# Kernel tuning notes

Hardware: AMD Instinct MI355X
Metric: run time of the kernel (lower is better)

Reference implementation:

```python
import jax, jax.numpy as jnp
import numpy as np

B, S, H = 2, 2048, 2048
NH, NKV, HD = 16, 4, 128
ROPE_BASE = 10000.0


def setup_inputs() -> dict:
    key = jax.random.key(0)
    ks = jax.random.split(key, 5)
    x = jax.random.normal(ks[0], (B, S, H), dtype=jnp.float32)
    position_ids = jnp.arange(S, dtype=jnp.int64 if jax.config.jax_enable_x64 else jnp.int32).reshape(1, S)
    # Linear weights stored as [in, out] (equivalent to torch weight.T)
    sc = 1.0 / np.sqrt(H)
    Wq = jax.random.normal(ks[1], (H, NH * HD), dtype=jnp.float32) * sc
    Wk = jax.random.normal(ks[2], (H, NKV * HD), dtype=jnp.float32) * sc
    Wv = jax.random.normal(ks[3], (H, NKV * HD), dtype=jnp.float32) * sc
    Wo = jax.random.normal(ks[4], (NH * HD, H), dtype=jnp.float32) * (1.0 / np.sqrt(NH * HD))
    return {"x": x, "position_ids": position_ids, "Wq": Wq, "Wk": Wk, "Wv": Wv, "Wo": Wo}


def _rope(q, k, position_ids):
    # q: [B,S,NH,HD], k: [B,S,NKV,HD]; Llama-style half-split RoPE
    half = HD // 2
    inv_freq = 1.0 / (ROPE_BASE ** (jnp.arange(0, half, dtype=jnp.float32) * 2.0 / HD))
    ang = position_ids.astype(jnp.float32)[..., None] * inv_freq  # [b,S,half]
    cos = jnp.concatenate([jnp.cos(ang), jnp.cos(ang)], axis=-1)[:, :, None, :]  # [b,S,1,HD]
    sin = jnp.concatenate([jnp.sin(ang), jnp.sin(ang)], axis=-1)[:, :, None, :]

    def rot_half(t):
        t1, t2 = t[..., :half], t[..., half:]
        return jnp.concatenate([-t2, t1], axis=-1)

    return q * cos + rot_half(q) * sin, k * cos + rot_half(k) * sin


def reference(x, position_ids, Wq, Wk, Wv, Wo):
    b, s, _ = x.shape
    q = (x @ Wq).reshape(b, s, NH, HD)
    k = (x @ Wk).reshape(b, s, NKV, HD)
    v = (x @ Wv).reshape(b, s, NKV, HD)
    q, k = _rope(q, k, position_ids)
    reps = NH // NKV
    k = jnp.repeat(k, reps, axis=2)  # repeat_interleave on head dim
    v = jnp.repeat(v, reps, axis=2)
    q = q.transpose(0, 2, 1, 3)  # [b,h,s,d]
    k = k.transpose(0, 2, 1, 3)
    v = v.transpose(0, 2, 1, 3)
    scores = jnp.einsum('bhqd,bhkd->bhqk', q, k) / jnp.sqrt(jnp.float32(HD))
    causal = jnp.triu(jnp.ones((s, s), dtype=bool), k=1)
    scores = jnp.where(causal, -jnp.inf, scores)
    attn = jax.nn.softmax(scores.astype(jnp.float32), axis=-1).astype(q.dtype)
    out = jnp.einsum('bhqk,bhkd->bhqd', attn, v)
    out = out.transpose(0, 2, 1, 3).reshape(b, s, NH * HD)
    return out @ Wo
```

## Files before the change

### kernel.cpp

```cpp
#include <hip/hip_runtime.h>
#include <stdint.h>

typedef unsigned short u16;
typedef __attribute__((ext_vector_type(8))) short short8;
typedef __attribute__((ext_vector_type(4))) float floatx4;

#define S_LEN 2048
#define NQKV 3072

#if __has_builtin(__builtin_amdgcn_exp2f)
#define EXP2F __builtin_amdgcn_exp2f
#else
#define EXP2F exp2f
#endif

__device__ inline float bf2f(u16 u) {
  union { uint32_t u; float f; } v; v.u = ((uint32_t)u) << 16; return v.f;
}
__device__ inline u16 f2bf(float f) {
  union { float f; uint32_t u; } v; v.f = f;
  uint32_t r = v.u + 0x7fffu + ((v.u >> 16) & 1u);
  return (u16)(r >> 16);
}
__device__ inline void gl2lds16(const u16* g, u16* l) {
  __builtin_amdgcn_global_load_lds((const __attribute__((address_space(1))) uint32_t*)g,
                                   (__attribute__((address_space(3))) uint32_t*)l, 16, 0, 0);
}

__global__ void cast_k(const float* __restrict__ in, u16* __restrict__ out, int n4) {
  int i = blockIdx.x * 256 + threadIdx.x;
  if (i >= n4) return;
  float4 v = ((const float4*)in)[i];
  ushort4 o;
  o.x = f2bf(v.x); o.y = f2bf(v.y); o.z = f2bf(v.z); o.w = f2bf(v.w);
  ((ushort4*)out)[i] = o;
}

__global__ void transpose_k(const float* __restrict__ in, u16* __restrict__ out, int K, int N) {
  __shared__ u16 tile[32][33];
  int n0 = blockIdx.x * 32, k0 = blockIdx.y * 32;
  int tx = threadIdx.x, ty = threadIdx.y;
#pragma unroll
  for (int i = 0; i < 4; i++)
    tile[ty + 8 * i][tx] = f2bf(in[(size_t)(k0 + ty + 8 * i) * N + n0 + tx]);
  __syncthreads();
#pragma unroll
  for (int i = 0; i < 4; i++)
    out[(size_t)(n0 + ty + 8 * i) * K + k0 + tx] = tile[tx][ty + 8 * i];
}

__global__ void vtrans_k(const u16* __restrict__ qkv, u16* __restrict__ vt) {
  __shared__ u16 tile[32][33];
  int bk = blockIdx.x * 32, bd = blockIdx.y * 32, bz = blockIdx.z;
  int bb = bz >> 2, kvh = bz & 3;
  const u16* src = qkv + ((size_t)bb * S_LEN) * NQKV + 2560 + kvh * 128;
  u16* dst = vt + (size_t)bz * 128 * 2048;
  int tx = threadIdx.x, ty = threadIdx.y;
#pragma unroll
  for (int i = 0; i < 4; i++)
    tile[ty + 8 * i][tx] = src[(size_t)(bk + ty + 8 * i) * NQKV + bd + tx];
  __syncthreads();
#pragma unroll
  for (int i = 0; i < 4; i++)
    dst[(size_t)(bd + ty + 8 * i) * 2048 + bk + tx] = tile[tx][ty + 8 * i];
}

template <bool OUTF32>
__global__ __launch_bounds__(256) void gemm_bt(const u16* __restrict__ A, const u16* __restrict__ Bt,
                                               void* __restrict__ Cv, int M, int N, int K) {
  __shared__ u16 As[128 * 32];
  __shared__ u16 Bs[128 * 32];
  const int m0 = blockIdx.y * 128, n0 = blockIdx.x * 128;
  const int t = threadIdx.x, w = t >> 6, lane = t & 63;
  const int quad = lane >> 4, l16 = lane & 15;
  const int wm = (w >> 1) * 64, wn = (w & 1) * 64;
  const int lrow = lane >> 2, lk = (lane & 3) * 8;
  floatx4 acc[4][4] = {};
  for (int k0 = 0; k0 < K; k0 += 32) {
#pragma unroll
    for (int c = 2 * w; c <= 2 * w + 1; ++c) {
      int row = c * 16 + lrow;
      gl2lds16(A + (size_t)(m0 + row) * K + k0 + lk, As + c * 512 + lane * 8);
      gl2lds16(Bt + (size_t)(n0 + row) * K + k0 + lk, Bs + c * 512 + lane * 8);
    }
    __syncthreads();
    short8 a[4], b[4];
#pragma unroll
    for (int mt = 0; mt < 4; mt++) a[mt] = *(const short8*)(As + (wm + mt * 16 + l16) * 32 + quad * 8);
#pragma unroll
    for (int nt = 0; nt < 4; nt++) b[nt] = *(const short8*)(Bs + (wn + nt * 16 + l16) * 32 + quad * 8);
#pragma unroll
    for (int mt = 0; mt < 4; mt++)
#pragma unroll
      for (int nt = 0; nt < 4; nt++)
        acc[mt][nt] = __builtin_amdgcn_mfma_f32_16x16x32_bf16(a[mt], b[nt], acc[mt][nt], 0, 0, 0);
    __syncthreads();
  }
#pragma unroll
  for (int mt = 0; mt < 4; mt++)
#pragma unroll
    for (int nt = 0; nt < 4; nt++)
#pragma unroll
      for (int r = 0; r < 4; r++) {
        int row = m0 + wm + mt * 16 + quad * 4 + r;
        int col = n0 + wn + nt * 16 + l16;
        if (OUTF32)
          ((float*)Cv)[(size_t)row * N + col] = acc[mt][nt][r];
        else
          ((u16*)Cv)[(size_t)row * N + col] = f2bf(acc[mt][nt][r]);
      }
}

__global__ __launch_bounds__(512, 2) void gemm256_k(const u16* __restrict__ A,
                                                    const u16* __restrict__ Bt,
                                                    u16* __restrict__ C, int N, int K) {
  __shared__ u16 Al[2][2][8192];
  __shared__ u16 Bl[2][2][8192];
  const int TN = N >> 8;
  int flat = blockIdx.x;
  const int cpx = gridDim.x >> 3;
  flat = (flat & 7) * cpx + (flat >> 3);
  const int m0 = (flat / TN) << 8, n0 = (flat % TN) << 8;
  const int t = threadIdx.x, w = t >> 6, lane = t & 63;
  const int quad = lane >> 4, l16 = lane & 15;
  const int wm = w >> 2, wn = w & 3;
  const int sr = t >> 3, sl = t & 7;
  floatx4 acc[2][2][4][2] = {};
  const int NKT = K >> 6;

  const int ra_l = wm * 64 + l16;
  const int rb_l = wn * 32 + l16;

#pragma unroll
  for (int round = 0; round < 2; round++) {
    int r = round * 64 + sr;
    int so = (sl ^ (r & 7)) << 3;
    gl2lds16(A + (size_t)(m0 + r) * K + so, &Al[0][0][0] + round * 4096 + t * 8);
    gl2lds16(Bt + (size_t)(n0 + r) * K + so, &Bl[0][0][0] + round * 4096 + t * 8);
    gl2lds16(Bt + (size_t)(n0 + 128 + r) * K + so, &Bl[0][1][0] + round * 4096 + t * 8);
    gl2lds16(A + (size_t)(m0 + 128 + r) * K + so, &Al[0][1][0] + round * 4096 + t * 8);
  }
  asm volatile("s_waitcnt vmcnt(0)" ::: "memory");
  __builtin_amdgcn_s_barrier();

  short8 af[4][2];
  short8 bf[2][2][2];

  for (int kt = 0; kt < NKT; kt++) {
    const int c = kt & 1;
    const u16* Ab = &Al[c][0][0];
    const u16* Bb = &Bl[c][0][0];
    u16* An = &Al[c ^ 1][0][0];
    u16* Bn = &Bl[c ^ 1][0][0];
    const int k1 = (kt + 1) << 6;
    const bool pf = (kt + 1 < NKT);
#pragma unroll
    for (int ph = 0; ph < 4; ph++) {
      const int mh = (ph >> 1);
      const int nh = (ph == 1 || ph == 2) ? 1 : 0;
      if (ph == 0 || ph == 2) {
#pragma unroll
        for (int mt = 0; mt < 4; mt++) {
          int ra = ra_l + mt * 16;
          const u16* base = Ab + mh * 8192 + ra * 64;
#pragma unroll
          for (int ks = 0; ks < 2; ks++)
            af[mt][ks] = *(const short8*)(base + (((ks * 4 + quad) ^ (ra & 7)) << 3));
        }
      }
      if (ph == 0 || ph == 1) {
#pragma unroll
        for (int nt = 0; nt < 2; nt++) {
          int rb = rb_l + nt * 16;
          const u16* base = Bb + nh * 8192 + rb * 64;
#pragma unroll
          for (int ks = 0; ks < 2; ks++)
            bf[nh][nt][ks] = *(const short8*)(base + (((ks * 4 + quad) ^ (rb & 7)) << 3));
        }
      }
      if (pf) {
        const u16* G;
        u16* L;
        int rbase;
        if (ph == 0)      { G = A;  L = An;        rbase = m0; }
        else if (ph == 1) { G = Bt; L = Bn;        rbase = n0; }
        else if (ph == 2) { G = Bt; L = Bn + 8192; rbase = n0 + 128; }
        else              { G = A;  L = An + 8192; rbase = m0 + 128; }
#pragma unroll
        for (int round = 0; round < 2; round++) {
          int r = round * 64 + sr;
          gl2lds16(G + (size_t)(rbase + r) * K + k1 + ((sl ^ (r & 7)) << 3),
                   L + round * 4096 + t * 8);
        }
      }
      __builtin_amdgcn_s_barrier();
      asm volatile("s_waitcnt lgkmcnt(0)" ::: "memory");
      __builtin_amdgcn_s_setprio(1);
#pragma unroll
      for (int mt = 0; mt < 4; mt++)
#pragma unroll
        for (int nt = 0; nt < 2; nt++)
#pragma unroll
          for (int ks = 0; ks < 2; ks++)
            acc[mh][nh][mt][nt] =
                __builtin_amdgcn_mfma_f32_16x16x32_bf16(af[mt][ks], bf[nh][nt][ks], acc[mh][nh][mt][nt], 0, 0, 0);
      __builtin_amdgcn_s_setprio(0);
      if (ph != 2) asm volatile("s_waitcnt vmcnt(4)" ::: "memory");
      __builtin_amdgcn_s_barrier();
    }
  }
#pragma unroll
  for (int mh = 0; mh < 2; mh++)
#pragma unroll
    for (int nh = 0; nh < 2; nh++)
#pragma unroll
      for (int mt = 0; mt < 4; mt++)
#pragma unroll
        for (int nt = 0; nt < 2; nt++)
#pragma unroll
          for (int r = 0; r < 4; r++) {
            int row = m0 + mh * 128 + wm * 64 + mt * 16 + quad * 4 + r;
            int col = n0 + nh * 128 + wn * 32 + nt * 16 + l16;
            C[(size_t)row * N + col] = f2bf(acc[mh][nh][mt][nt][r]);
          }
}

__global__ void rope_k(u16* __restrict__ qkv, const int* __restrict__ pos) {
  int idx = blockIdx.x * 256 + threadIdx.x;
  int i = idx & 63;
  int hh = (idx >> 6) % 20;
  int row = idx / (64 * 20);
  int s = row & (S_LEN - 1);
  float p = (float)pos[s];
  float freq = __expf(-(float)i * 0.015625f * 9.210340371976184f);
  float ang = p * freq;
  float c = cosf(ang), sn = sinf(ang);
  int col = (hh < 16) ? hh * 128 : 2048 + (hh - 16) * 128;
  size_t base = (size_t)row * NQKV + col + i;
  float t1 = bf2f(qkv[base]), t2 = bf2f(qkv[base + 64]);
  qkv[base] = f2bf(t1 * c - t2 * sn);
  qkv[base + 64] = f2bf(t2 * c + t1 * sn);
}

__global__ __launch_bounds__(256) void attn_k(const u16* __restrict__ qkv,
                                              const u16* __restrict__ vt,
                                              u16* __restrict__ ctx) {
  __shared__ u16 Kl[2][64 * 128];
  __shared__ u16 Vl[2][128 * 64];
  const int p = blockIdx.x;
  const int h = blockIdx.y, bb = blockIdx.z;
  const int kvh = h >> 2;
  const int t = threadIdx.x, w = t >> 6, lane = t & 63;
  const int quad = lane >> 4, l16 = lane & 15;
  const int sx = l16 & 7;
  const int kslot = lane & 15;
  const int vd0 = w * 32 + (lane >> 3);
  const int vslot = lane & 7;
  const int grow0 = (w & 1) * 4 + (w >> 1) * 32 + quad;
  const size_t rowbase = (size_t)bb * S_LEN;
  const u16* Kg0 = qkv + rowbase * NQKV + 2048 + kvh * 128;
  const u16* Vg0 = vt + (size_t)(bb * 4 + kvh) * 128 * 2048;
  const float c2 = 0.12751744f;
  short8 onesf = {16256, 16256, 16256, 16256, 16256, 16256, 16256, 16256};

  for (int phase = 0; phase < 2; phase++) {
    const int qt = phase ? p : 31 - p;
    const int rw = qt * 64 + w * 16;
    const int qrow = rw + l16;

    short8 qf[4];
#pragma unroll
    for (int ks = 0; ks < 4; ks++)
      qf[ks] = *(const short8*)(qkv + (rowbase + rw + l16) * NQKV + h * 128 + ks * 32 + quad * 8);

    floatx4 acc[8] = {};
    floatx4 accl = {0.f, 0.f, 0.f, 0.f};

    __syncthreads();
    {
      const u16* Kg = Kg0;
      const u16* Vg = Vg0;
#pragma unroll
      for (int ii = 0; ii < 4; ii++) {
        int p7 = (quad + 4 * ii) & 7;
        int grow = grow0 + 8 * ii;
        gl2lds16(Kg + (size_t)grow * NQKV + ((kslot ^ p7) * 8),
                 &Kl[0][0] + w * 2048 + ii * 512 + lane * 8);
      }
#pragma unroll
      for (int ii = 0; ii < 4; ii++) {
        int d = vd0 + ii * 8;
        gl2lds16(Vg + (size_t)d * 2048 + ((vslot ^ (d & 7)) * 8),
                 &Vl[0][0] + w * 2048 + ii * 512 + lane * 8);
      }
    }

    for (int kb = 0; kb <= qt; kb++) {
      const int cur = kb & 1;
      __syncthreads();
      if (kb < qt) {
        const u16* Kg = Kg0 + (size_t)(kb + 1) * 64 * NQKV;
        const u16* Vg = Vg0 + (kb + 1) * 64;
        u16* KlN = &Kl[cur ^ 1][0];
        u16* VlN = &Vl[cur ^ 1][0];
#pragma unroll
        for (int ii = 0; ii < 4; ii++) {
          int p7 = (quad + 4 * ii) & 7;
          int grow = grow0 + 8 * ii;
          gl2lds16(Kg + (size_t)grow * NQKV + ((kslot ^ p7) * 8),
                   KlN + w * 2048 + ii * 512 + lane * 8);
        }
#pragma unroll
        for (int ii = 0; ii < 4; ii++) {
          int d = vd0 + ii * 8;
          gl2lds16(Vg + (size_t)d * 2048 + ((vslot ^ (d & 7)) * 8),
                   VlN + w * 2048 + ii * 512 + lane * 8);
        }
      }
      const u16* KlB = &Kl[cur][0];
      const u16* VlB = &Vl[cur][0];

      floatx4 sc[4];
#pragma unroll
      for (int nt = 0; nt < 4; nt++) {
        const u16* Krow = KlB + (nt * 16 + l16) * 128;
        short8 kf[4];
#pragma unroll
        for (int ks = 0; ks < 4; ks++)
          kf[ks] = *(const short8*)(Krow + (((ks * 4 + quad) ^ sx) * 8));
        floatx4 s = {0.f, 0.f, 0.f, 0.f};
#pragma unroll
        for (int ks = 0; ks < 4; ks++) s = __builtin_amdgcn_mfma_f32_16x16x32_bf16(kf[ks], qf[ks], s, 0, 0, 0);
        sc[nt] = s;
      }
      const bool diag = (kb == qt);
      uint32_t pw[8];
#pragma unroll
      for (int nt = 0; nt < 4; nt++) {
        uint32_t w0 = 0, w1 = 0;
#pragma unroll
        for (int r = 0; r < 4; r++) {
          float e = EXP2F(sc[nt][r] * c2);
          if (diag) {
            int keyg = kb * 64 + quad * 8 + (nt & 1) * 4 + (nt >> 1) * 32 + r;
            if (keyg > qrow) e = 0.f;
          }
          uint32_t b = __float_as_uint(e) >> 16;
          if (r == 0) w0 = b;
          else if (r == 1) w0 |= b << 16;
          else if (r == 2) w1 = b;
          else w1 |= b << 16;
        }
        pw[nt * 2] = w0;
        pw[nt * 2 + 1] = w1;
      }
      union { short8 v; uint32_t u[4]; } pu0, pu1;
      pu0.u[0] = pw[0]; pu0.u[1] = pw[1]; pu0.u[2] = pw[2]; pu0.u[3] = pw[3];
      pu1.u[0] = pw[4]; pu1.u[1] = pw[5]; pu1.u[2] = pw[6]; pu1.u[3] = pw[7];
      const short8 pf0 = pu0.v, pf1 = pu1.v;

      accl = __builtin_amdgcn_mfma_f32_16x16x32_bf16(pf0, onesf, accl, 0, 0, 0);
      accl = __builtin_amdgcn_mfma_f32_16x16x32_bf16(pf1, onesf, accl, 0, 0, 0);
#pragma unroll
      for (int nto = 0; nto < 8; nto++) {
        const u16* Vrow = VlB + (nto * 16 + l16) * 64;
        short8 vf0 = *(const short8*)(Vrow + ((quad ^ sx) * 8));
        short8 vf1 = *(const short8*)(Vrow + (((quad + 4) ^ sx) * 8));
        acc[nto] = __builtin_amdgcn_mfma_f32_16x16x32_bf16(pf0, vf0, acc[nto], 0, 0, 0);
        acc[nto] = __builtin_amdgcn_mfma_f32_16x16x32_bf16(pf1, vf1, acc[nto], 0, 0, 0);
      }
    }
#pragma unroll
    for (int r = 0; r < 4; r++) {
      float inv = 1.0f / accl[r];
      int rowg = rw + quad * 4 + r;
#pragma unroll
      for (int nto = 0; nto < 8; nto++) {
        int col = h * 128 + nto * 16 + l16;
        ctx[(rowbase + rowg) * 2048 + col] = f2bf(acc[nto][r] * inv);
      }
    }
  }
}

extern "C" void kernel_launch(void* const* d_in, const int* in_sizes, int n_in,
                              void* d_out, int out_size, void* d_ws, size_t ws_size,
                              hipStream_t stream) {
  const float* x  = (const float*)d_in[0];
  const int* pos  = (const int*)d_in[1];
  const float* Wq = (const float*)d_in[2];
  const float* Wk = (const float*)d_in[3];
  const float* Wv = (const float*)d_in[4];
  const float* Wo = (const float*)d_in[5];
  float* out = (float*)d_out;
  char* ws = (char*)d_ws;
  u16* Xb  = (u16*)(ws);
  u16* WT  = (u16*)(ws + 16777216);
  u16* WoT = (u16*)(ws + 29360128);
  u16* QKV = (u16*)(ws + 37748736);
  u16* CTX = (u16*)(ws + 62914560);
  u16* VT  = Xb;

  hipLaunchKernelGGL(cast_k, dim3(8192), dim3(256), 0, stream, x, Xb, 2097152);

  dim3 tb(32, 8);
  hipLaunchKernelGGL(transpose_k, dim3(64, 64), tb, 0, stream, Wq, WT, 2048, 2048);
  hipLaunchKernelGGL(transpose_k, dim3(16, 64), tb, 0, stream, Wk, WT + (size_t)2048 * 2048, 2048, 512);
  hipLaunchKernelGGL(transpose_k, dim3(16, 64), tb, 0, stream, Wv, WT + (size_t)2560 * 2048, 2048, 512);
  hipLaunchKernelGGL(transpose_k, dim3(64, 64), tb, 0, stream, Wo, WoT, 2048, 2048);

  hipLaunchKernelGGL(gemm256_k, dim3(192), dim3(512), 0, stream, Xb, WT, QKV, 3072, 2048);
  hipLaunchKernelGGL(rope_k, dim3(20480), dim3(256), 0, stream, QKV, pos);
  hipLaunchKernelGGL(vtrans_k, dim3(64, 4, 8), tb, 0, stream, QKV, VT);
  hipLaunchKernelGGL(attn_k, dim3(16, 16, 2), dim3(256), 0, stream, QKV, VT, CTX);
  hipLaunchKernelGGL(HIP_KERNEL_NAME(gemm_bt<true>), dim3(16, 32), dim3(256), 0, stream,
                     CTX, WoT, (void*)out, 4096, 2048, 2048);
}
```

Measured before the change: 304.1 us.

## Reschedule 256-tile GEMM fragment loads and merge weight transpose launches

The QKV GEMM main loop is restructured so each k-step loads all B fragments and the first A half up front. It then runs the four quadrant MFMA groups in a snake order (00, 01, 11, 10), reusing the A and B register fragments across quadrants and interleaving the next-tile global-to-LDS prefetches with explicit barriers and vmcnt waits. The aim is to cut LDS reads and lgkm stalls between phases, at the cost of more live registers. Separately, the four weight-transpose launches are merged into one 3D-grid kernel, with early exit for the narrower K/V matrices, to reduce launch overhead.

```diff
diff --git a/kernel.cpp b/kernel.cpp
--- a/kernel.cpp
+++ b/kernel.cpp
@@ -36,17 +36,26 @@
   ((ushort4*)out)[i] = o;
 }
 
-__global__ void transpose_k(const float* __restrict__ in, u16* __restrict__ out, int K, int N) {
+__global__ void wtrans_k(const float* __restrict__ Wq, const float* __restrict__ Wk,
+                         const float* __restrict__ Wv, const float* __restrict__ Wo,
+                         u16* __restrict__ WT, u16* __restrict__ WoT) {
   __shared__ u16 tile[32][33];
+  const int z = blockIdx.z;
+  const float* src; u16* dst; int N;
+  if (z == 0)      { src = Wq; dst = WT;                       N = 2048; }
+  else if (z == 1) { src = Wk; dst = WT + (size_t)2048 * 2048; N = 512;  }
+  else if (z == 2) { src = Wv; dst = WT + (size_t)2560 * 2048; N = 512;  }
+  else             { src = Wo; dst = WoT;                      N = 2048; }
   int n0 = blockIdx.x * 32, k0 = blockIdx.y * 32;
+  if (n0 >= N) return;
   int tx = threadIdx.x, ty = threadIdx.y;
 #pragma unroll
   for (int i = 0; i < 4; i++)
-    tile[ty + 8 * i][tx] = f2bf(in[(size_t)(k0 + ty + 8 * i) * N + n0 + tx]);
+    tile[ty + 8 * i][tx] = f2bf(src[(size_t)(k0 + ty + 8 * i) * N + n0 + tx]);
   __syncthreads();
 #pragma unroll
   for (int i = 0; i < 4; i++)
-    out[(size_t)(n0 + ty + 8 * i) * K + k0 + tx] = tile[tx][ty + 8 * i];
+    dst[(size_t)(n0 + ty + 8 * i) * 2048 + k0 + tx] = tile[tx][ty + 8 * i];
 }
 
 __global__ void vtrans_k(const u16* __restrict__ qkv, u16* __restrict__ vt) {
@@ -143,9 +152,6 @@
   asm volatile("s_waitcnt vmcnt(0)" ::: "memory");
   __builtin_amdgcn_s_barrier();
 
-  short8 af[4][2];
-  short8 bf[2][2][2];
-
   for (int kt = 0; kt < NKT; kt++) {
     const int c = kt & 1;
     const u16* Ab = &Al[c][0][0];
@@ -154,60 +160,119 @@
     u16* Bn = &Bl[c ^ 1][0][0];
     const int k1 = (kt + 1) << 6;
     const bool pf = (kt + 1 < NKT);
-#pragma unroll
-    for (int ph = 0; ph < 4; ph++) {
-      const int mh = (ph >> 1);
-      const int nh = (ph == 1 || ph == 2) ? 1 : 0;
-      if (ph == 0 || ph == 2) {
-#pragma unroll
-        for (int mt = 0; mt < 4; mt++) {
-          int ra = ra_l + mt * 16;
-          const u16* base = Ab + mh * 8192 + ra * 64;
-#pragma unroll
-          for (int ks = 0; ks < 2; ks++)
-            af[mt][ks] = *(const short8*)(base + (((ks * 4 + quad) ^ (ra & 7)) << 3));
-        }
-      }
-      if (ph == 0 || ph == 1) {
-#pragma unroll
-        for (int nt = 0; nt < 2; nt++) {
-          int rb = rb_l + nt * 16;
-          const u16* base = Bb + nh * 8192 + rb * 64;
-#pragma unroll
-          for (int ks = 0; ks < 2; ks++)
-            bf[nh][nt][ks] = *(const short8*)(base + (((ks * 4 + quad) ^ (rb & 7)) << 3));
-        }
-      }
-      if (pf) {
-        const u16* G;
-        u16* L;
-        int rbase;
-        if (ph == 0)      { G = A;  L = An;        rbase = m0; }
-        else if (ph == 1) { G = Bt; L = Bn;        rbase = n0; }
-        else if (ph == 2) { G = Bt; L = Bn + 8192; rbase = n0 + 128; }
-        else              { G = A;  L = An + 8192; rbase = m0 + 128; }
-#pragma unroll
-        for (int round = 0; round < 2; round++) {
-          int r = round * 64 + sr;
-          gl2lds16(G + (size_t)(rbase + r) * K + k1 + ((sl ^ (r & 7)) << 3),
-                   L + round * 4096 + t * 8);
-        }
-      }
-      __builtin_amdgcn_s_barrier();
-      asm volatile("s_waitcnt lgkmcnt(0)" ::: "memory");
-      __builtin_amdgcn_s_setprio(1);
-#pragma unroll
-      for (int mt = 0; mt < 4; mt++)
-#pragma unroll
-        for (int nt = 0; nt < 2; nt++)
-#pragma unroll
-          for (int ks = 0; ks < 2; ks++)
-            acc[mh][nh][mt][nt] =
-                __builtin_amdgcn_mfma_f32_16x16x32_bf16(af[mt][ks], bf[nh][nt][ks], acc[mh][nh][mt][nt], 0, 0, 0);
-      __builtin_amdgcn_s_setprio(0);
-      if (ph != 2) asm volatile("s_waitcnt vmcnt(4)" ::: "memory");
-      __builtin_amdgcn_s_barrier();
-    }
+
+    short8 afA[4][2], afB[4][2], bfr[2][2][2];
+
+    if (pf) {
+#pragma unroll
+      for (int round = 0; round < 2; round++) {
+        int r = round * 64 + sr;
+        gl2lds16(A + (size_t)(m0 + r) * K + k1 + ((sl ^ (r & 7)) << 3), An + round * 4096 + t * 8);
+      }
+    }
+#pragma unroll
+    for (int mt = 0; mt < 4; mt++) {
+      int ra = ra_l + mt * 16;
+      const u16* base = Ab + ra * 64;
+#pragma unroll
+      for (int ks = 0; ks < 2; ks++)
+        afA[mt][ks] = *(const short8*)(base + (((ks * 4 + quad) ^ (ra & 7)) << 3));
+    }
+#pragma unroll
+    for (int nh = 0; nh < 2; nh++)
+#pragma unroll
+      for (int nt = 0; nt < 2; nt++) {
+        int rb = rb_l + nt * 16;
+        const u16* base = Bb + nh * 8192 + rb * 64;
+#pragma unroll
+        for (int ks = 0; ks < 2; ks++)
+          bfr[nh][nt][ks] = *(const short8*)(base + (((ks * 4 + quad) ^ (rb & 7)) << 3));
+      }
+    __builtin_amdgcn_s_barrier();
+    __builtin_amdgcn_s_setprio(1);
+#pragma unroll
+    for (int mt = 0; mt < 4; mt++)
+#pragma unroll
+      for (int nt = 0; nt < 2; nt++)
+#pragma unroll
+        for (int ks = 0; ks < 2; ks++)
+          acc[0][0][mt][nt] =
+              __builtin_amdgcn_mfma_f32_16x16x32_bf16(afA[mt][ks], bfr[0][nt][ks], acc[0][0][mt][nt], 0, 0, 0);
+    __builtin_amdgcn_s_setprio(0);
+    if (pf) asm volatile("s_waitcnt vmcnt(2)" ::: "memory");
+    else    asm volatile("s_waitcnt vmcnt(0)" ::: "memory");
+    __builtin_amdgcn_s_barrier();
+
+    if (pf) {
+#pragma unroll
+      for (int round = 0; round < 2; round++) {
+        int r = round * 64 + sr;
+        gl2lds16(Bt + (size_t)(n0 + r) * K + k1 + ((sl ^ (r & 7)) << 3), Bn + round * 4096 + t * 8);
+      }
+    }
+#pragma unroll
+    for (int mt = 0; mt < 4; mt++) {
+      int ra = ra_l + mt * 16;
+      const u16* base = Ab + 8192 + ra * 64;
+#pragma unroll
+      for (int ks = 0; ks < 2; ks++)
+        afB[mt][ks] = *(const short8*)(base + (((ks * 4 + quad) ^ (ra & 7)) << 3));
+    }
+    __builtin_amdgcn_s_barrier();
+    __builtin_amdgcn_s_setprio(1);
+#pragma unroll
+    for (int mt = 0; mt < 4; mt++)
+#pragma unroll
+      for (int nt = 0; nt < 2; nt++)
+#pragma unroll
+        for (int ks = 0; ks < 2; ks++)
+          acc[0][1][mt][nt] =
+              __builtin_amdgcn_mfma_f32_16x16x32_bf16(afA[mt][ks], bfr[1][nt][ks], acc[0][1][mt][nt], 0, 0, 0);
+    __builtin_amdgcn_s_setprio(0);
+    __builtin_amdgcn_s_barrier();
+
+    if (pf) {
+#pragma unroll
+      for (int round = 0; round < 2; round++) {
+        int r = round * 64 + sr;
+        gl2lds16(Bt + (size_t)(n0 + 128 + r) * K + k1 + ((sl ^ (r & 7)) << 3),
+                 Bn + 8192 + round * 4096 + t * 8);
+      }
+    }
+    __builtin_amdgcn_s_barrier();
+    __builtin_amdgcn_s_setprio(1);
+#pragma unroll
+    for (int mt = 0; mt < 4; mt++)
+#pragma unroll
+      for (int nt = 0; nt < 2; nt++)
+#pragma unroll
+        for (int ks = 0; ks < 2; ks++)
+          acc[1][1][mt][nt] =
+              __builtin_amdgcn_mfma_f32_16x16x32_bf16(afB[mt][ks], bfr[1][nt][ks], acc[1][1][mt][nt], 0, 0, 0);
+    __builtin_amdgcn_s_setprio(0);
+    __builtin_amdgcn_s_barrier();
+
+    if (pf) {
+#pragma unroll
+      for (int round = 0; round < 2; round++) {
+        int r = round * 64 + sr;
+        gl2lds16(A + (size_t)(m0 + 128 + r) * K + k1 + ((sl ^ (r & 7)) << 3),
+                 An + 8192 + round * 4096 + t * 8);
+      }
+    }
+    __builtin_amdgcn_s_barrier();
+    __builtin_amdgcn_s_setprio(1);
+#pragma unroll
+    for (int mt = 0; mt < 4; mt++)
+#pragma unroll
+      for (int nt = 0; nt < 2; nt++)
+#pragma unroll
+        for (int ks = 0; ks < 2; ks++)
+          acc[1][0][mt][nt] =
+              __builtin_amdgcn_mfma_f32_16x16x32_bf16(afB[mt][ks], bfr[0][nt][ks], acc[1][0][mt][nt], 0, 0, 0);
+    __builtin_amdgcn_s_setprio(0);
+    if (pf) asm volatile("s_waitcnt vmcnt(2)" ::: "memory");
+    __builtin_amdgcn_s_barrier();
   }
 #pragma unroll
   for (int mh = 0; mh < 2; mh++)
@@ -404,10 +469,7 @@
   hipLaunchKernelGGL(cast_k, dim3(8192), dim3(256), 0, stream, x, Xb, 2097152);
 
   dim3 tb(32, 8);
-  hipLaunchKernelGGL(transpose_k, dim3(64, 64), tb, 0, stream, Wq, WT, 2048, 2048);
-  hipLaunchKernelGGL(transpose_k, dim3(16, 64), tb, 0, stream, Wk, WT + (size_t)2048 * 2048, 2048, 512);
-  hipLaunchKernelGGL(transpose_k, dim3(16, 64), tb, 0, stream, Wv, WT + (size_t)2560 * 2048, 2048, 512);
-  hipLaunchKernelGGL(transpose_k, dim3(64, 64), tb, 0, stream, Wo, WoT, 2048, 2048);
+  hipLaunchKernelGGL(wtrans_k, dim3(64, 64, 4), tb, 0, stream, Wq, Wk, Wv, Wo, WT, WoT);
 
   hipLaunchKernelGGL(gemm256_k, dim3(192), dim3(512), 0, stream, Xb, WT, QKV, 3072, 2048);
   hipLaunchKernelGGL(rope_k, dim3(20480), dim3(256), 0, stream, QKV, pos);
```

Result: slower. 318.8 us (+4.8%).

## Double attention query tile to 128 rows and merge weight transposes into one launch

Applied to the files above, without the earlier changes.

The attention kernel now gives each block a 128-row query tile, with each wave holding two 16-row query fragments. Every K/V tile loaded into LDS is therefore reused for twice as many queries, which halves the grid and the K/V traffic per query. Waves whose rows lie entirely before a key block skip its compute, and the causal mask is applied whenever the block overlaps the diagonal. The four weight-transpose launches are merged into one launch that picks its source by z-index, trading more registers per thread and fewer blocks for less launch overhead.

```diff
diff --git a/kernel.cpp b/kernel.cpp
--- a/kernel.cpp
+++ b/kernel.cpp
@@ -36,17 +36,26 @@
   ((ushort4*)out)[i] = o;
 }
 
-__global__ void transpose_k(const float* __restrict__ in, u16* __restrict__ out, int K, int N) {
+__global__ void wtrans_k(const float* __restrict__ Wq, const float* __restrict__ Wk,
+                         const float* __restrict__ Wv, const float* __restrict__ Wo,
+                         u16* __restrict__ WT, u16* __restrict__ WoT) {
   __shared__ u16 tile[32][33];
+  const int z = blockIdx.z;
+  const float* src; u16* dst; int N;
+  if (z == 0)      { src = Wq; dst = WT;                       N = 2048; }
+  else if (z == 1) { src = Wk; dst = WT + (size_t)2048 * 2048; N = 512;  }
+  else if (z == 2) { src = Wv; dst = WT + (size_t)2560 * 2048; N = 512;  }
+  else             { src = Wo; dst = WoT;                      N = 2048; }
   int n0 = blockIdx.x * 32, k0 = blockIdx.y * 32;
+  if (n0 >= N) return;
   int tx = threadIdx.x, ty = threadIdx.y;
 #pragma unroll
   for (int i = 0; i < 4; i++)
-    tile[ty + 8 * i][tx] = f2bf(in[(size_t)(k0 + ty + 8 * i) * N + n0 + tx]);
+    tile[ty + 8 * i][tx] = f2bf(src[(size_t)(k0 + ty + 8 * i) * N + n0 + tx]);
   __syncthreads();
 #pragma unroll
   for (int i = 0; i < 4; i++)
-    out[(size_t)(n0 + ty + 8 * i) * K + k0 + tx] = tile[tx][ty + 8 * i];
+    dst[(size_t)(n0 + ty + 8 * i) * 2048 + k0 + tx] = tile[tx][ty + 8 * i];
 }
 
 __global__ void vtrans_k(const u16* __restrict__ qkv, u16* __restrict__ vt) {
@@ -264,17 +273,19 @@
   short8 onesf = {16256, 16256, 16256, 16256, 16256, 16256, 16256, 16256};
 
   for (int phase = 0; phase < 2; phase++) {
-    const int qt = phase ? p : 31 - p;
-    const int rw = qt * 64 + w * 16;
-    const int qrow = rw + l16;
-
-    short8 qf[4];
-#pragma unroll
-    for (int ks = 0; ks < 4; ks++)
-      qf[ks] = *(const short8*)(qkv + (rowbase + rw + l16) * NQKV + h * 128 + ks * 32 + quad * 8);
-
-    floatx4 acc[8] = {};
-    floatx4 accl = {0.f, 0.f, 0.f, 0.f};
+    const int qt = phase ? p : 15 - p;
+    const int rw = qt * 128 + w * 32;
+    const int nkb = 2 * (qt + 1);
+
+    short8 qf[2][4];
+#pragma unroll
+    for (int qh = 0; qh < 2; qh++)
+#pragma unroll
+      for (int ks = 0; ks < 4; ks++)
+        qf[qh][ks] = *(const short8*)(qkv + (rowbase + rw + qh * 16 + l16) * NQKV + h * 128 + ks * 32 + quad * 8);
+
+    floatx4 acc[2][8] = {};
+    floatx4 accl[2] = {};
 
     __syncthreads();
     {
@@ -295,10 +306,10 @@
       }
     }
 
-    for (int kb = 0; kb <= qt; kb++) {
+    for (int kb = 0; kb < nkb; kb++) {
       const int cur = kb & 1;
       __syncthreads();
-      if (kb < qt) {
+      if (kb + 1 < nkb) {
         const u16* Kg = Kg0 + (size_t)(kb + 1) * 64 * NQKV;
         const u16* Vg = Vg0 + (kb + 1) * 64;
         u16* KlN = &Kl[cur ^ 1][0];
@@ -317,10 +328,11 @@
                    VlN + w * 2048 + ii * 512 + lane * 8);
         }
       }
+      if (kb * 64 > rw + 31) continue;
       const u16* KlB = &Kl[cur][0];
       const u16* VlB = &Vl[cur][0];
 
-      floatx4 sc[4];
+      floatx4 sc[2][4];
 #pragma unroll
       for (int nt = 0; nt < 4; nt++) {
         const u16* Krow = KlB + (nt * 16 + l16) * 128;
@@ -328,58 +340,70 @@
 #pragma unroll
         for (int ks = 0; ks < 4; ks++)
           kf[ks] = *(const short8*)(Krow + (((ks * 4 + quad) ^ sx) * 8));
-        floatx4 s = {0.f, 0.f, 0.f, 0.f};
-#pragma unroll
-        for (int ks = 0; ks < 4; ks++) s = __builtin_amdgcn_mfma_f32_16x16x32_bf16(kf[ks], qf[ks], s, 0, 0, 0);
-        sc[nt] = s;
-      }
-      const bool diag = (kb == qt);
-      uint32_t pw[8];
-#pragma unroll
-      for (int nt = 0; nt < 4; nt++) {
-        uint32_t w0 = 0, w1 = 0;
-#pragma unroll
-        for (int r = 0; r < 4; r++) {
-          float e = EXP2F(sc[nt][r] * c2);
-          if (diag) {
-            int keyg = kb * 64 + quad * 8 + (nt & 1) * 4 + (nt >> 1) * 32 + r;
-            if (keyg > qrow) e = 0.f;
+#pragma unroll
+        for (int qh = 0; qh < 2; qh++) {
+          floatx4 s = {0.f, 0.f, 0.f, 0.f};
+#pragma unroll
+          for (int ks = 0; ks < 4; ks++) s = __builtin_amdgcn_mfma_f32_16x16x32_bf16(kf[ks], qf[qh][ks], s, 0, 0, 0);
+          sc[qh][nt] = s;
+        }
+      }
+      const bool diag = (kb * 64 + 63) > rw;
+      short8 pfr[2][2];
+#pragma unroll
+      for (int qh = 0; qh < 2; qh++) {
+        const int qrow = rw + qh * 16 + l16;
+        uint32_t pw[8];
+#pragma unroll
+        for (int nt = 0; nt < 4; nt++) {
+          uint32_t w0 = 0, w1 = 0;
+#pragma unroll
+          for (int r = 0; r < 4; r++) {
+            float e = EXP2F(sc[qh][nt][r] * c2);
+            if (diag) {
+              int keyg = kb * 64 + quad * 8 + (nt & 1) * 4 + (nt >> 1) * 32 + r;
+              if (keyg > qrow) e = 0.f;
+            }
+            uint32_t b = __float_as_uint(e) >> 16;
+            if (r == 0) w0 = b;
+            else if (r == 1) w0 |= b << 16;
+            else if (r == 2) w1 = b;
+            else w1 |= b << 16;
           }
-          uint32_t b = __float_as_uint(e) >> 16;
-          if (r == 0) w0 = b;
-          else if (r == 1) w0 |= b << 16;
-          else if (r == 2) w1 = b;
-          else w1 |= b << 16;
-        }
-        pw[nt * 2] = w0;
-        pw[nt * 2 + 1] = w1;
-      }
-      union { short8 v; uint32_t u[4]; } pu0, pu1;
-      pu0.u[0] = pw[0]; pu0.u[1] = pw[1]; pu0.u[2] = pw[2]; pu0.u[3] = pw[3];
-      pu1.u[0] = pw[4]; pu1.u[1] = pw[5]; pu1.u[2] = pw[6]; pu1.u[3] = pw[7];
-      const short8 pf0 = pu0.v, pf1 = pu1.v;
-
-      accl = __builtin_amdgcn_mfma_f32_16x16x32_bf16(pf0, onesf, accl, 0, 0, 0);
-      accl = __builtin_amdgcn_mfma_f32_16x16x32_bf16(pf1, onesf, accl, 0, 0, 0);
+          pw[nt * 2] = w0;
+          pw[nt * 2 + 1] = w1;
+        }
+        union { short8 v; uint32_t u[4]; } pu0, pu1;
+        pu0.u[0] = pw[0]; pu0.u[1] = pw[1]; pu0.u[2] = pw[2]; pu0.u[3] = pw[3];
+        pu1.u[0] = pw[4]; pu1.u[1] = pw[5]; pu1.u[2] = pw[6]; pu1.u[3] = pw[7];
+        pfr[qh][0] = pu0.v; pfr[qh][1] = pu1.v;
+        accl[qh] = __builtin_amdgcn_mfma_f32_16x16x32_bf16(pfr[qh][0], onesf, accl[qh], 0, 0, 0);
+        accl[qh] = __builtin_amdgcn_mfma_f32_16x16x32_bf16(pfr[qh][1], onesf, accl[qh], 0, 0, 0);
+      }
 #pragma unroll
       for (int nto = 0; nto < 8; nto++) {
         const u16* Vrow = VlB + (nto * 16 + l16) * 64;
         short8 vf0 = *(const short8*)(Vrow + ((quad ^ sx) * 8));
         short8 vf1 = *(const short8*)(Vrow + (((quad + 4) ^ sx) * 8));
-        acc[nto] = __builtin_amdgcn_mfma_f32_16x16x32_bf16(pf0, vf0, acc[nto], 0, 0, 0);
-        acc[nto] = __builtin_amdgcn_mfma_f32_16x16x32_bf16(pf1, vf1, acc[nto], 0, 0, 0);
+#pragma unroll
+        for (int qh = 0; qh < 2; qh++) {
+          acc[qh][nto] = __builtin_amdgcn_mfma_f32_16x16x32_bf16(pfr[qh][0], vf0, acc[qh][nto], 0, 0, 0);
+          acc[qh][nto] = __builtin_amdgcn_mfma_f32_16x16x32_bf16(pfr[qh][1], vf1, acc[qh][nto], 0, 0, 0);
+        }
       }
     }
 #pragma unroll
-    for (int r = 0; r < 4; r++) {
-      float inv = 1.0f / accl[r];
-      int rowg = rw + quad * 4 + r;
-#pragma unroll
-      for (int nto = 0; nto < 8; nto++) {
-        int col = h * 128 + nto * 16 + l16;
-        ctx[(rowbase + rowg) * 2048 + col] = f2bf(acc[nto][r] * inv);
-      }
-    }
+    for (int qh = 0; qh < 2; qh++)
+#pragma unroll
+      for (int r = 0; r < 4; r++) {
+        float inv = 1.0f / accl[qh][r];
+        int rowg = rw + qh * 16 + quad * 4 + r;
+#pragma unroll
+        for (int nto = 0; nto < 8; nto++) {
+          int col = h * 128 + nto * 16 + l16;
+          ctx[(rowbase + rowg) * 2048 + col] = f2bf(acc[qh][nto][r] * inv);
+        }
+      }
   }
 }
 
@@ -404,15 +428,12 @@
   hipLaunchKernelGGL(cast_k, dim3(8192), dim3(256), 0, stream, x, Xb, 2097152);
 
   dim3 tb(32, 8);
-  hipLaunchKernelGGL(transpose_k, dim3(64, 64), tb, 0, stream, Wq, WT, 2048, 2048);
-  hipLaunchKernelGGL(transpose_k, dim3(16, 64), tb, 0, stream, Wk, WT + (size_t)2048 * 2048, 2048, 512);
-  hipLaunchKernelGGL(transpose_k, dim3(16, 64), tb, 0, stream, Wv, WT + (size_t)2560 * 2048, 2048, 512);
-  hipLaunchKernelGGL(transpose_k, dim3(64, 64), tb, 0, stream, Wo, WoT, 2048, 2048);
+  hipLaunchKernelGGL(wtrans_k, dim3(64, 64, 4), tb, 0, stream, Wq, Wk, Wv, Wo, WT, WoT);
 
   hipLaunchKernelGGL(gemm256_k, dim3(192), dim3(512), 0, stream, Xb, WT, QKV, 3072, 2048);
   hipLaunchKernelGGL(rope_k, dim3(20480), dim3(256), 0, stream, QKV, pos);
   hipLaunchKernelGGL(vtrans_k, dim3(64, 4, 8), tb, 0, stream, QKV, VT);
-  hipLaunchKernelGGL(attn_k, dim3(16, 16, 2), dim3(256), 0, stream, QKV, VT, CTX);
+  hipLaunchKernelGGL(attn_k, dim3(8, 16, 2), dim3(256), 0, stream, QKV, VT, CTX);
   hipLaunchKernelGGL(HIP_KERNEL_NAME(gemm_bt<true>), dim3(16, 32), dim3(256), 0, stream,
                      CTX, WoT, (void*)out, 4096, 2048, 2048);
 }
```

New measurement: 324.8 us. 6.8% more time.

## Fuse RoPE into QKV GEMM epilogue and merge prep kernels into one launch

Applied to the files above, without the earlier changes.

The cast and four weight transposes are merged into a single prep kernel, cutting launch count. The QKV GEMM's B-fragment column mapping is remapped so each thread holds columns d and d+64 of a head. This lets RoPE be applied in the epilogue before storing, which removes the separate rope kernel's read-modify-write pass over Q and K. In exchange, each epilogue row computes sin/cos, which adds transcendental work inside the GEMM.

```diff
diff --git a/kernel.cpp b/kernel.cpp
--- a/kernel.cpp
+++ b/kernel.cpp
@@ -27,26 +27,36 @@
                                    (__attribute__((address_space(3))) uint32_t*)l, 16, 0, 0);
 }
 
-__global__ void cast_k(const float* __restrict__ in, u16* __restrict__ out, int n4) {
-  int i = blockIdx.x * 256 + threadIdx.x;
-  if (i >= n4) return;
-  float4 v = ((const float4*)in)[i];
-  ushort4 o;
-  o.x = f2bf(v.x); o.y = f2bf(v.y); o.z = f2bf(v.z); o.w = f2bf(v.w);
-  ((ushort4*)out)[i] = o;
-}
-
-__global__ void transpose_k(const float* __restrict__ in, u16* __restrict__ out, int K, int N) {
+__global__ void prep_k(const float* __restrict__ x, u16* __restrict__ Xb,
+                       const float* __restrict__ Wq, const float* __restrict__ Wk,
+                       const float* __restrict__ Wv, const float* __restrict__ Wo,
+                       u16* __restrict__ WT, u16* __restrict__ WoT) {
   __shared__ u16 tile[32][33];
-  int n0 = blockIdx.x * 32, k0 = blockIdx.y * 32;
-  int tx = threadIdx.x, ty = threadIdx.y;
+  const int b = blockIdx.x, t = threadIdx.x;
+  if (b < 8192) {
+    int i = b * 256 + t;
+    float4 v = ((const float4*)x)[i];
+    ushort4 o;
+    o.x = f2bf(v.x); o.y = f2bf(v.y); o.z = f2bf(v.z); o.w = f2bf(v.w);
+    ((ushort4*)Xb)[i] = o;
+    return;
+  }
+  int wb = b - 8192;
+  const float* src; u16* dst; int bx, by;
+  if (wb < 4096)      { src = Wq; dst = WT;                       bx = wb & 63;  by = wb >> 6; }
+  else if (wb < 5120) { src = Wk; dst = WT + (size_t)2048 * 2048; bx = (wb - 4096) & 15; by = (wb - 4096) >> 4; }
+  else if (wb < 6144) { src = Wv; dst = WT + (size_t)2560 * 2048; bx = (wb - 5120) & 15; by = (wb - 5120) >> 4; }
+  else                { src = Wo; dst = WoT;                      bx = (wb - 6144) & 63; by = (wb - 6144) >> 6; }
+  const int N = (wb >= 4096 && wb < 6144) ? 512 : 2048;
+  int n0 = bx * 32, k0 = by * 32;
+  int tx = t & 31, ty = t >> 5;
 #pragma unroll
   for (int i = 0; i < 4; i++)
-    tile[ty + 8 * i][tx] = f2bf(in[(size_t)(k0 + ty + 8 * i) * N + n0 + tx]);
+    tile[ty + 8 * i][tx] = f2bf(src[(size_t)(k0 + ty + 8 * i) * N + n0 + tx]);
   __syncthreads();
 #pragma unroll
   for (int i = 0; i < 4; i++)
-    out[(size_t)(n0 + ty + 8 * i) * K + k0 + tx] = tile[tx][ty + 8 * i];
+    dst[(size_t)(n0 + ty + 8 * i) * 2048 + k0 + tx] = tile[tx][ty + 8 * i];
 }
 
 __global__ void vtrans_k(const u16* __restrict__ qkv, u16* __restrict__ vt) {
@@ -113,7 +123,9 @@
 
 __global__ __launch_bounds__(512, 2) void gemm256_k(const u16* __restrict__ A,
                                                     const u16* __restrict__ Bt,
-                                                    u16* __restrict__ C, int N, int K) {
+                                                    u16* __restrict__ C,
+                                                    const int* __restrict__ pos,
+                                                    int N, int K) {
   __shared__ u16 Al[2][2][8192];
   __shared__ u16 Bl[2][2][8192];
   const int TN = N >> 8;
@@ -129,7 +141,7 @@
   const int NKT = K >> 6;
 
   const int ra_l = wm * 64 + l16;
-  const int rb_l = wn * 32 + l16;
+  const int rb_l = wn * 16 + l16;
 
 #pragma unroll
   for (int round = 0; round < 2; round++) {
@@ -171,7 +183,7 @@
       if (ph == 0 || ph == 1) {
 #pragma unroll
         for (int nt = 0; nt < 2; nt++) {
-          int rb = rb_l + nt * 16;
+          int rb = rb_l + nt * 64;
           const u16* base = Bb + nh * 8192 + rb * 64;
 #pragma unroll
           for (int ks = 0; ks < 2; ks++)
@@ -209,37 +221,30 @@
       __builtin_amdgcn_s_barrier();
     }
   }
+  const bool dorope = (n0 < 2560);
+  const float rfreq = __expf(-(float)(wn * 16 + l16) * 0.015625f * 9.210340371976184f);
 #pragma unroll
   for (int mh = 0; mh < 2; mh++)
 #pragma unroll
-    for (int nh = 0; nh < 2; nh++)
-#pragma unroll
-      for (int mt = 0; mt < 4; mt++)
-#pragma unroll
-        for (int nt = 0; nt < 2; nt++)
-#pragma unroll
-          for (int r = 0; r < 4; r++) {
-            int row = m0 + mh * 128 + wm * 64 + mt * 16 + quad * 4 + r;
-            int col = n0 + nh * 128 + wn * 32 + nt * 16 + l16;
-            C[(size_t)row * N + col] = f2bf(acc[mh][nh][mt][nt][r]);
-          }
-}
-
-__global__ void rope_k(u16* __restrict__ qkv, const int* __restrict__ pos) {
-  int idx = blockIdx.x * 256 + threadIdx.x;
-  int i = idx & 63;
-  int hh = (idx >> 6) % 20;
-  int row = idx / (64 * 20);
-  int s = row & (S_LEN - 1);
-  float p = (float)pos[s];
-  float freq = __expf(-(float)i * 0.015625f * 9.210340371976184f);
-  float ang = p * freq;
-  float c = cosf(ang), sn = sinf(ang);
-  int col = (hh < 16) ? hh * 128 : 2048 + (hh - 16) * 128;
-  size_t base = (size_t)row * NQKV + col + i;
-  float t1 = bf2f(qkv[base]), t2 = bf2f(qkv[base + 64]);
-  qkv[base] = f2bf(t1 * c - t2 * sn);
-  qkv[base + 64] = f2bf(t2 * c + t1 * sn);
+    for (int mt = 0; mt < 4; mt++)
+#pragma unroll
+      for (int r = 0; r < 4; r++) {
+        int row = m0 + mh * 128 + wm * 64 + mt * 16 + quad * 4 + r;
+        float cc = 1.f, sn = 0.f;
+        if (dorope) {
+          float ang = (float)pos[row & (S_LEN - 1)] * rfreq;
+          cc = cosf(ang); sn = sinf(ang);
+        }
+#pragma unroll
+        for (int nh = 0; nh < 2; nh++) {
+          float a0 = acc[mh][nh][mt][0][r], a1 = acc[mh][nh][mt][1][r];
+          float o0 = dorope ? (a0 * cc - a1 * sn) : a0;
+          float o1 = dorope ? (a1 * cc + a0 * sn) : a1;
+          int colb = n0 + nh * 128 + wn * 16 + l16;
+          C[(size_t)row * N + colb]      = f2bf(o0);
+          C[(size_t)row * N + colb + 64] = f2bf(o1);
+        }
+      }
 }
 
 __global__ __launch_bounds__(256) void attn_k(const u16* __restrict__ qkv,
@@ -401,16 +406,10 @@
   u16* CTX = (u16*)(ws + 62914560);
   u16* VT  = Xb;
 
-  hipLaunchKernelGGL(cast_k, dim3(8192), dim3(256), 0, stream, x, Xb, 2097152);
-
+  hipLaunchKernelGGL(prep_k, dim3(18432), dim3(256), 0, stream, x, Xb, Wq, Wk, Wv, Wo, WT, WoT);
+
+  hipLaunchKernelGGL(gemm256_k, dim3(192), dim3(512), 0, stream, Xb, WT, QKV, pos, 3072, 2048);
   dim3 tb(32, 8);
-  hipLaunchKernelGGL(transpose_k, dim3(64, 64), tb, 0, stream, Wq, WT, 2048, 2048);
-  hipLaunchKernelGGL(transpose_k, dim3(16, 64), tb, 0, stream, Wk, WT + (size_t)2048 * 2048, 2048, 512);
-  hipLaunchKernelGGL(transpose_k, dim3(16, 64), tb, 0, stream, Wv, WT + (size_t)2560 * 2048, 2048, 512);
-  hipLaunchKernelGGL(transpose_k, dim3(64, 64), tb, 0, stream, Wo, WoT, 2048, 2048);
-
-  hipLaunchKernelGGL(gemm256_k, dim3(192), dim3(512), 0, stream, Xb, WT, QKV, 3072, 2048);
-  hipLaunchKernelGGL(rope_k, dim3(20480), dim3(256), 0, stream, QKV, pos);
   hipLaunchKernelGGL(vtrans_k, dim3(64, 4, 8), tb, 0, stream, QKV, VT);
   hipLaunchKernelGGL(attn_k, dim3(16, 16, 2), dim3(256), 0, stream, QKV, VT, CTX);
   hipLaunchKernelGGL(HIP_KERNEL_NAME(gemm_bt<true>), dim3(16, 32), dim3(256), 0, stream,
```

New measurement: 296.4 us. 1.03x faster.
